# Kernel optimization log

Measured on AMD Instinct MI355X. Metric: run time of the kernel, lower is better.

## Reference

```python
import jax, jax.numpy as jnp
import numpy as np

N_NODES = 50000
N_EDGES = 640000
D = 128
BN_EPS = 1e-5
NEG_SLOPE = 0.2  # PyG GATv2Conv default negative_slope


def setup_inputs() -> dict:
    key = jax.random.key(0)
    ks = jax.random.split(key, 8)
    s = 1.0 / np.sqrt(D)
    x = jax.random.normal(ks[0], (N_NODES, D), dtype=jnp.float32)
    edge_index = jax.random.randint(ks[1], (2, N_EDGES), 0, N_NODES, dtype=jnp.int32)
    edge_attr = jax.random.uniform(ks[2], (N_EDGES, 1), dtype=jnp.float32)
    Wl = jax.random.normal(ks[3], (D, D), dtype=jnp.float32) * s
    Wr = jax.random.normal(ks[4], (D, D), dtype=jnp.float32) * s
    We = jax.random.normal(ks[5], (1, D), dtype=jnp.float32) * s
    att = jax.random.normal(ks[6], (D,), dtype=jnp.float32) * s
    return {
        "x": x, "edge_index": edge_index, "edge_attr": edge_attr,
        "Wl": Wl, "bl": jnp.zeros((D,), jnp.float32),
        "Wr": Wr, "br": jnp.zeros((D,), jnp.float32),
        "We": We, "att": att,
        "bias_out": jnp.zeros((D,), jnp.float32),
        "bn_gamma": jnp.ones((D,), jnp.float32),
        "bn_beta": jnp.zeros((D,), jnp.float32),
    }


def _gatv2(x, edge_index, edge_attr, Wl, bl, Wr, br, We, att, bias_out):
    # GATv2Conv, heads=1, concat=True, dropout treated as eval (p=0)
    src, dst = edge_index[0], edge_index[1]
    xl = x @ Wl + bl                      # source-side transform [N, D]
    xr = x @ Wr + br                      # target-side transform [N, D]
    e = edge_attr @ We                    # edge embedding       [E, D]
    m = xl[src] + xr[dst] + e             # gather + fuse        [E, D]
    m = jax.nn.leaky_relu(m, NEG_SLOPE)
    logits = m @ att                      # per-edge score [E]
    n = x.shape[0]
    # segment softmax over destination node neighborhoods
    mx = jax.ops.segment_max(logits, dst, num_segments=n)
    ex = jnp.exp(logits - mx[dst])
    den = jax.ops.segment_sum(ex, dst, num_segments=n)
    alpha = ex / (den[dst] + 1e-16)
    out = jax.ops.segment_sum(xl[src] * alpha[:, None], dst, num_segments=n)
    return out + bias_out


def reference(x, edge_index, edge_attr, Wl, bl, Wr, br, We, att, bias_out,
              bn_gamma, bn_beta):
    h = x + _gatv2(x, edge_index, edge_attr, Wl, bl, Wr, br, We, att, bias_out)
    h = jax.nn.gelu(h, approximate=False)  # torch nn.GELU default (erf)
    # BatchNorm over node dim, training-style batch stats (biased var)
    mean = jnp.mean(h, axis=0)
    var = jnp.mean((h - mean) ** 2, axis=0)
    h = (h - mean) * jax.lax.rsqrt(var + BN_EPS) * bn_gamma + bn_beta
    return h
```

## Files before the change

### kernel.cpp

```cpp
#include <hip/hip_runtime.h>
#include <math.h>

#define D 128
#define SCAN_CHUNK 256

typedef __attribute__((ext_vector_type(8))) short short8;
typedef __attribute__((ext_vector_type(4))) float f32x4;

__device__ __forceinline__ unsigned short f2bf(float f) {
    unsigned u = __float_as_uint(f);
    unsigned r = (u + 0x7fff + ((u >> 16) & 1)) >> 16;
    return (unsigned short)r;
}
__device__ __forceinline__ float bflo(unsigned u) { return __uint_as_float(u << 16); }
__device__ __forceinline__ float bfhi(unsigned u) { return __uint_as_float(u & 0xffff0000u); }

__global__ __launch_bounds__(256) void init_pack_k(const float* __restrict__ Wl,
    const float* __restrict__ Wr, unsigned short* __restrict__ wpack,
    int* __restrict__ deg, int* __restrict__ deghist, int n, int nzb)
{
    if (blockIdx.x < 16) {
        const int lane = threadIdx.x & 63;
        const int wv = threadIdx.x >> 6;
        const int slot = blockIdx.x * 4 + wv;
        const int ct = slot >> 2;
        const int kt = slot & 3;
        const float* W = (ct < 8) ? Wl : Wr;
        const int cb = (ct & 7) * 16 + (lane & 15);
        const int kb = kt * 32 + (lane >> 4) * 8;
        unsigned short v[8];
#pragma unroll
        for (int i = 0; i < 8; i++) v[i] = f2bf(W[(size_t)(kb + i) * D + cb]);
        *(uint4*)(wpack + ((size_t)slot << 9) + lane * 8) = *(uint4*)v;
    } else {
        const int tid = (blockIdx.x - 16) * 256 + threadIdx.x;
        const int stride = nzb * 256;
        for (int i = tid; i < n; i += stride) deg[i] = 0;
        if (tid < 256) deghist[tid] = 0;
    }
}

__global__ __launch_bounds__(256) void gemm_mfma_k(const float* __restrict__ x,
    const unsigned short* __restrict__ wpack, const float* __restrict__ bl,
    const float* __restrict__ br, unsigned* __restrict__ xlb,
    float* __restrict__ xr, int n)
{
    const int lane = threadIdx.x & 63;
    const int wv = threadIdx.x >> 6;
    const int rt = blockIdx.x * 4 + wv;
    if (rt * 16 >= n) return;
    const int r0 = rt * 16;
    const int ra = r0 + (lane & 15);
    const int r = ra < n ? ra : n - 1;
    const int ko = (lane >> 4) * 8;

    short8 a[4];
#pragma unroll
    for (int kt = 0; kt < 4; kt++) {
        const float* px = x + (size_t)r * D + kt * 32 + ko;
        float4 lo = *(const float4*)px;
        float4 hi = *(const float4*)(px + 4);
        short8 t;
        t[0] = (short)f2bf(lo.x); t[1] = (short)f2bf(lo.y);
        t[2] = (short)f2bf(lo.z); t[3] = (short)f2bf(lo.w);
        t[4] = (short)f2bf(hi.x); t[5] = (short)f2bf(hi.y);
        t[6] = (short)f2bf(hi.z); t[7] = (short)f2bf(hi.w);
        a[kt] = t;
    }

    f32x4 acc[16];
#pragma unroll
    for (int i = 0; i < 16; i++) acc[i] = (f32x4){0.f, 0.f, 0.f, 0.f};

#pragma unroll
    for (int kt = 0; kt < 4; kt++) {
#pragma unroll
        for (int ct = 0; ct < 16; ct++) {
            short8 b = *(const short8*)(wpack + (((size_t)(ct * 4 + kt)) << 9) + lane * 8);
            acc[ct] = __builtin_amdgcn_mfma_f32_16x16x32_bf16(a[kt], b, acc[ct], 0, 0, 0);
        }
    }

    const int colb = lane & 15;
    const int rbase = r0 + (lane >> 4) * 4;
#pragma unroll
    for (int ct = 8; ct < 16; ct++) {
        const int c = (ct - 8) * 16 + colb;
        const float bb = br[c];
#pragma unroll
        for (int reg = 0; reg < 4; reg++) {
            const int row = rbase + reg;
            if (row < n) xr[(size_t)row * D + c] = acc[ct][reg] + bb;
        }
    }
#pragma unroll
    for (int ct = 0; ct < 8; ct++) {
        const int c = ct * 16 + colb;
        const float bb = bl[c];
#pragma unroll
        for (int reg = 0; reg < 4; reg++) {
            unsigned mybf = f2bf(acc[ct][reg] + bb);
            unsigned other = (unsigned)__shfl_xor((int)mybf, 1);
            if ((lane & 1) == 0) {
                const int row = rbase + reg;
                if (row < n) xlb[(size_t)row * 64 + (c >> 1)] = mybf | (other << 16);
            }
        }
    }
}

__global__ __launch_bounds__(256) void hist_k(const int* __restrict__ ei,
    int* __restrict__ deg, int E)
{
    const int tid = blockIdx.x * 256 + threadIdx.x;
    const int stride = gridDim.x * 256;
#pragma unroll
    for (int u = 0; u < 4; u++) {
        const int e = tid + u * stride;
        if (e < E) atomicAdd(&deg[ei[E + e]], 1);
    }
}

__global__ __launch_bounds__(256) void scan_sum_k(const int* __restrict__ deg,
    int* __restrict__ bsum, int* __restrict__ deghist, int n)
{
    __shared__ int lh[256];
    const int t = threadIdx.x;
    lh[t] = 0;
    __syncthreads();
    const int i = blockIdx.x * SCAN_CHUNK + t;
    int s = 0;
    if (i < n) {
        s = deg[i];
        atomicAdd(&lh[min(s, 255)], 1);
    }
#pragma unroll
    for (int off = 32; off > 0; off >>= 1) s += __shfl_xor(s, off);
    __shared__ int ws_[4];
    const int lane = t & 63, w = t >> 6;
    if (lane == 0) ws_[w] = s;
    __syncthreads();
    if (t == 0) bsum[blockIdx.x] = ws_[0] + ws_[1] + ws_[2] + ws_[3];
    if (lh[t]) atomicAdd(&deghist[t], lh[t]);
}

__global__ __launch_bounds__(256) void scan_off_k(const int* __restrict__ bsum,
    int* __restrict__ boff, int* __restrict__ rowptr,
    const int* __restrict__ deghist, int* __restrict__ degcur, int nb, int n)
{
    const int t = threadIdx.x;
    const int lane = t & 63, w = t >> 6;
    int v = (t < nb) ? bsum[t] : 0;
    int inc = v;
#pragma unroll
    for (int off = 1; off < 64; off <<= 1) {
        int u = __shfl_up(inc, off);
        if (lane >= off) inc += u;
    }
    __shared__ int wsum[4], wpre[4];
    if (lane == 63) wsum[w] = inc;
    __syncthreads();
    if (t == 0) {
        int r = 0;
#pragma unroll
        for (int j = 0; j < 4; j++) { wpre[j] = r; r += wsum[j]; }
        rowptr[n] = r;
    }
    __syncthreads();
    if (t < nb) boff[t] = inc - v + wpre[w];
    int dv = deghist[t];
    int dinc = dv;
#pragma unroll
    for (int off = 1; off < 64; off <<= 1) {
        int u = __shfl_up(dinc, off);
        if (lane >= off) dinc += u;
    }
    __shared__ int w2sum[4], w2pre[4];
    if (lane == 63) w2sum[w] = dinc;
    __syncthreads();
    if (t == 0) {
        int r = 0;
#pragma unroll
        for (int j = 0; j < 4; j++) { w2pre[j] = r; r += w2sum[j]; }
    }
    __syncthreads();
    degcur[t] = dinc - dv + w2pre[w];
}

__global__ __launch_bounds__(256) void scan_fin_k(int* __restrict__ deg,
    const int* __restrict__ boff, int* __restrict__ rowptr,
    int* __restrict__ degcur, int* __restrict__ nodeord, int n)
{
    __shared__ int wsum[4], wpre[4];
    __shared__ int lh[256], lbase[256];
    const int t = threadIdx.x;
    const int i = blockIdx.x * SCAN_CHUNK + t;
    lh[t] = 0;
    int v = (i < n) ? deg[i] : 0;
    const int bin = min(v, 255);
    const int lane = t & 63, w = t >> 6;
    int inc = v;
#pragma unroll
    for (int off = 1; off < 64; off <<= 1) {
        int u = __shfl_up(inc, off);
        if (lane >= off) inc += u;
    }
    if (lane == 63) wsum[w] = inc;
    __syncthreads();
    if (t == 0) {
        int r = 0;
#pragma unroll
        for (int j = 0; j < 4; j++) { wpre[j] = r; r += wsum[j]; }
    }
    __syncthreads();
    int rank = 0;
    if (i < n) {
        rank = atomicAdd(&lh[bin], 1);
        int ex = inc - v + wpre[w] + boff[blockIdx.x];
        rowptr[i] = ex;
        deg[i] = ex;
    }
    __syncthreads();
    lbase[t] = lh[t] ? atomicAdd(&degcur[t], lh[t]) : 0;
    __syncthreads();
    if (i < n) nodeord[lbase[bin] + rank] = i;
}

__global__ __launch_bounds__(256) void scatter_k(const int* __restrict__ ei,
    const float* __restrict__ ea, int* __restrict__ cursor,
    unsigned* __restrict__ edges, int E)
{
    const int tid = blockIdx.x * 256 + threadIdx.x;
    const int stride = gridDim.x * 256;
#pragma unroll
    for (int u = 0; u < 4; u++) {
        const int e = tid + u * stride;
        if (e < E) {
            const int dst = ei[E + e];
            const int pos = atomicAdd(&cursor[dst], 1);
            edges[pos] = ((unsigned)ei[e] << 16) | (unsigned)f2bf(ea[e]);
        }
    }
}

__global__ __launch_bounds__(256) void agg_k(const unsigned* __restrict__ xlb,
    const float* __restrict__ xr, const float* __restrict__ x,
    const float* __restrict__ bias, const int* __restrict__ rowptr,
    const unsigned* __restrict__ edges, const float* __restrict__ We,
    const float* __restrict__ att, const int* __restrict__ nodeord,
    unsigned* __restrict__ hbf, float* __restrict__ partials, int n)
{
    const int t = threadIdx.x;
    const int gg = (blockIdx.x * 256 + t) >> 4;
    const int li = t & 15;
    const int f0 = li * 8;
    const bool active = gg < n;

    float sum[8], sq[8];
#pragma unroll
    for (int k = 0; k < 8; k++) { sum[k] = 0.f; sq[k] = 0.f; }

    if (active) {
        const int v = nodeord[n - 1 - gg];
        const int beg = rowptr[v];
        const int end = rowptr[v + 1];

        float xrv[8], wev[8], atv[8];
        {
            float4 a0 = *(const float4*)(xr + (size_t)v * D + f0);
            float4 a1 = *(const float4*)(xr + (size_t)v * D + f0 + 4);
            xrv[0]=a0.x; xrv[1]=a0.y; xrv[2]=a0.z; xrv[3]=a0.w;
            xrv[4]=a1.x; xrv[5]=a1.y; xrv[6]=a1.z; xrv[7]=a1.w;
            float4 w0 = *(const float4*)(We + f0);
            float4 w1 = *(const float4*)(We + f0 + 4);
            wev[0]=w0.x; wev[1]=w0.y; wev[2]=w0.z; wev[3]=w0.w;
            wev[4]=w1.x; wev[5]=w1.y; wev[6]=w1.z; wev[7]=w1.w;
            float4 t0 = *(const float4*)(att + f0);
            float4 t1 = *(const float4*)(att + f0 + 4);
            atv[0]=t0.x; atv[1]=t0.y; atv[2]=t0.z; atv[3]=t0.w;
            atv[4]=t1.x; atv[5]=t1.y; atv[6]=t1.z; atv[7]=t1.w;
        }

        float m = -1e30f, s = 0.f;
        float acc[8];
#pragma unroll
        for (int k = 0; k < 8; k++) acc[k] = 0.f;

        int j = beg;
        unsigned pk0 = 0u, pk1 = 0u;
        uint4 xb0 = make_uint4(0,0,0,0), xb1 = make_uint4(0,0,0,0);
        if (j < end) {
            pk0 = edges[j];
            const int j1 = (j + 1 < end) ? j + 1 : end - 1;
            pk1 = edges[j1];
            xb0 = *(const uint4*)(xlb + (size_t)(pk0 >> 16) * 64 + li * 4);
            xb1 = *(const uint4*)(xlb + (size_t)(pk1 >> 16) * 64 + li * 4);
        }
        while (j < end) {
            const int jn = j + 2;
            unsigned pn0 = pk0, pn1 = pk1;
            uint4 xn0 = xb0, xn1 = xb1;
            if (jn < end) {
                pn0 = edges[jn];
                const int j3 = (jn + 1 < end) ? jn + 1 : end - 1;
                pn1 = edges[j3];
                xn0 = *(const uint4*)(xlb + (size_t)(pn0 >> 16) * 64 + li * 4);
                xn1 = *(const uint4*)(xlb + (size_t)(pn1 >> 16) * 64 + li * 4);
            }

            const float ea0 = bflo(pk0);
            const float ea1 = bflo(pk1);
            float xv0[8], xv1[8];
            xv0[0] = bflo(xb0.x); xv0[1] = bfhi(xb0.x);
            xv0[2] = bflo(xb0.y); xv0[3] = bfhi(xb0.y);
            xv0[4] = bflo(xb0.z); xv0[5] = bfhi(xb0.z);
            xv0[6] = bflo(xb0.w); xv0[7] = bfhi(xb0.w);
            xv1[0] = bflo(xb1.x); xv1[1] = bfhi(xb1.x);
            xv1[2] = bflo(xb1.y); xv1[3] = bfhi(xb1.y);
            xv1[4] = bflo(xb1.z); xv1[5] = bfhi(xb1.z);
            xv1[6] = bflo(xb1.w); xv1[7] = bfhi(xb1.w);

            float p0 = 0.f, p1 = 0.f;
#pragma unroll
            for (int k = 0; k < 8; k++) {
                float t0 = fmaf(ea0, wev[k], xrv[k]) + xv0[k];
                t0 = fmaxf(t0, 0.2f * t0);
                p0 = fmaf(t0, atv[k], p0);
                float t1 = fmaf(ea1, wev[k], xrv[k]) + xv1[k];
                t1 = fmaxf(t1, 0.2f * t1);
                p1 = fmaf(t1, atv[k], p1);
            }
#pragma unroll
            for (int off = 8; off >= 1; off >>= 1) {
                p0 += __shfl_xor(p0, off);
                p1 += __shfl_xor(p1, off);
            }
            if (j + 1 >= end) p1 = -1e30f;

            const float pm = fmaxf(m, fmaxf(p0, p1));
            const float sc = __expf(m - pm);
            const float w0 = __expf(p0 - pm);
            const float w1 = __expf(p1 - pm);
            s = s * sc + w0 + w1;
#pragma unroll
            for (int k = 0; k < 8; k++)
                acc[k] = fmaf(acc[k], sc, fmaf(w0, xv0[k], w1 * xv1[k]));
            m = pm;

            pk0 = pn0; pk1 = pn1; xb0 = xn0; xb1 = xn1; j = jn;
        }

        const float inv = 1.f / (s + 1e-16f);
        float xa[8], bb[8];
        {
            float4 a0 = *(const float4*)(x + (size_t)v * D + f0);
            float4 a1 = *(const float4*)(x + (size_t)v * D + f0 + 4);
            xa[0]=a0.x; xa[1]=a0.y; xa[2]=a0.z; xa[3]=a0.w;
            xa[4]=a1.x; xa[5]=a1.y; xa[6]=a1.z; xa[7]=a1.w;
            float4 b0 = *(const float4*)(bias + f0);
            float4 b1 = *(const float4*)(bias + f0 + 4);
            bb[0]=b0.x; bb[1]=b0.y; bb[2]=b0.z; bb[3]=b0.w;
            bb[4]=b1.x; bb[5]=b1.y; bb[6]=b1.z; bb[7]=b1.w;
        }
        float ge[8];
#pragma unroll
        for (int k = 0; k < 8; k++) {
            const float hv = xa[k] + fmaf(acc[k], inv, bb[k]);
            const float g = 0.5f * hv * (1.f + erff(hv * 0.70710678118654752f));
            ge[k] = g;
            sum[k] = g;
            sq[k] = g * g;
        }
        unsigned o0 = (unsigned)f2bf(ge[0]) | ((unsigned)f2bf(ge[1]) << 16);
        unsigned o1 = (unsigned)f2bf(ge[2]) | ((unsigned)f2bf(ge[3]) << 16);
        unsigned o2 = (unsigned)f2bf(ge[4]) | ((unsigned)f2bf(ge[5]) << 16);
        unsigned o3 = (unsigned)f2bf(ge[6]) | ((unsigned)f2bf(ge[7]) << 16);
        *(uint4*)(hbf + (size_t)v * 64 + li * 4) = make_uint4(o0, o1, o2, o3);
    }

#pragma unroll
    for (int k = 0; k < 8; k++) {
        sum[k] += __shfl_xor(sum[k], 16);
        sum[k] += __shfl_xor(sum[k], 32);
        sq[k]  += __shfl_xor(sq[k], 16);
        sq[k]  += __shfl_xor(sq[k], 32);
    }
    __shared__ float redS[4][128], redQ[4][128];
    const int wv_ = t >> 6;
    const int lane_ = t & 63;
    if (lane_ < 16) {
#pragma unroll
        for (int k = 0; k < 8; k++) {
            redS[wv_][f0 + k] = sum[k];
            redQ[wv_][f0 + k] = sq[k];
        }
    }
    __syncthreads();
    if (t < 128) {
        const float ts = redS[0][t] + redS[1][t] + redS[2][t] + redS[3][t];
        const float tq = redQ[0][t] + redQ[1][t] + redQ[2][t] + redQ[3][t];
        partials[(size_t)blockIdx.x * 256 + t] = ts;
        partials[(size_t)blockIdx.x * 256 + 128 + t] = tq;
    }
}

__global__ __launch_bounds__(256) void bn_reduce_params_k(const float* __restrict__ partials,
    const float* __restrict__ gamma, const float* __restrict__ beta,
    float* __restrict__ ab, float n, int nblk)
{
    const int c = blockIdx.x;
    const int t = threadIdx.x;
    float s = 0.f, q = 0.f;
    for (int b = t; b < nblk; b += 256) {
        s += partials[(size_t)b * 256 + c];
        q += partials[(size_t)b * 256 + 128 + c];
    }
#pragma unroll
    for (int off = 32; off > 0; off >>= 1) {
        s += __shfl_xor(s, off);
        q += __shfl_xor(q, off);
    }
    __shared__ float ss[4], qq[4];
    const int lane = t & 63, w = t >> 6;
    if (lane == 0) { ss[w] = s; qq[w] = q; }
    __syncthreads();
    if (t == 0) {
        float S = ss[0] + ss[1] + ss[2] + ss[3];
        float Q = qq[0] + qq[1] + qq[2] + qq[3];
        float mean = S / n;
        float var = Q / n - mean * mean;
        float a = rsqrtf(var + 1e-5f) * gamma[c];
        ab[c] = a;
        ab[c + 128] = beta[c] - mean * a;
    }
}

__global__ __launch_bounds__(256) void bn_apply_k(const unsigned* __restrict__ hbf,
    float* __restrict__ out, const float* __restrict__ ab, int total4)
{
    int i4 = blockIdx.x * blockDim.x + threadIdx.x;
    if (i4 >= total4) return;
    int cg = i4 & 31;
    uint2 hp = *(const uint2*)(hbf + (size_t)i4 * 2);
    float4 a = ((const float4*)ab)[cg];
    float4 b = ((const float4*)(ab + 128))[cg];
    ((float4*)out)[i4] = make_float4(bflo(hp.x) * a.x + b.x, bfhi(hp.x) * a.y + b.y,
                                     bflo(hp.y) * a.z + b.z, bfhi(hp.y) * a.w + b.w);
}

extern "C" void kernel_launch(void* const* d_in, const int* in_sizes, int n_in,
                              void* d_out, int out_size, void* d_ws, size_t ws_size,
                              hipStream_t stream)
{
    const float* x    = (const float*)d_in[0];
    const int*   ei   = (const int*)d_in[1];
    const float* ea   = (const float*)d_in[2];
    const float* Wl   = (const float*)d_in[3];
    const float* bl   = (const float*)d_in[4];
    const float* Wr   = (const float*)d_in[5];
    const float* br   = (const float*)d_in[6];
    const float* We   = (const float*)d_in[7];
    const float* att  = (const float*)d_in[8];
    const float* bias = (const float*)d_in[9];
    const float* gamma= (const float*)d_in[10];
    const float* beta = (const float*)d_in[11];
    float* out = (float*)d_out;

    const int n = in_sizes[0] / D;
    const int E = in_sizes[1] / 2;
    const int nb = (n + SCAN_CHUNK - 1) / SCAN_CHUNK;
    const int ablk = (n * 16 + 255) / 256;

    char* ws = (char*)d_ws;
    unsigned short* wpack = (unsigned short*)ws;
    unsigned* xlb = (unsigned*)(ws + 65536);
    unsigned* hbf = xlb + (size_t)n * 64;
    float* xr = (float*)(hbf + (size_t)n * 64);
    int* deg = (int*)(xr + (size_t)n * D);
    int* rowptr = deg + n;
    int* deghist = rowptr + n + 1;
    int* degcur = deghist + 256;
    int* nodeord = degcur + 256;
    int* bsum = nodeord + n;
    int* boff = bsum + nb;
    unsigned* edges = (unsigned*)(boff + nb);
    float* partials = (float*)(edges + E);
    float* ab = partials + (size_t)256 * ablk;

    const int nzb = 98;
    init_pack_k<<<16 + nzb, 256, 0, stream>>>(Wl, Wr, wpack, deg, deghist, n, nzb);
    const int nrt = (n + 15) / 16;
    gemm_mfma_k<<<(nrt + 3) / 4, 256, 0, stream>>>(x, wpack, bl, br, xlb, xr, n);
    hist_k<<<(E / 4 + 255) / 256, 256, 0, stream>>>(ei, deg, E);
    scan_sum_k<<<nb, 256, 0, stream>>>(deg, bsum, deghist, n);
    scan_off_k<<<1, 256, 0, stream>>>(bsum, boff, rowptr, deghist, degcur, nb, n);
    scan_fin_k<<<nb, 256, 0, stream>>>(deg, boff, rowptr, degcur, nodeord, n);
    scatter_k<<<(E / 4 + 255) / 256, 256, 0, stream>>>(ei, ea, deg, edges, E);
    agg_k<<<ablk, 256, 0, stream>>>(xlb, xr, x, bias, rowptr, edges, We, att,
                                    nodeord, hbf, partials, n);
    bn_reduce_params_k<<<128, 256, 0, stream>>>(partials, gamma, beta, ab, (float)n, ablk);
    const int total4 = (n * D) / 4;
    bn_apply_k<<<(total4 + 255) / 256, 256, 0, stream>>>(hbf, out, ab, total4);
}
```

Before: 181.0 us.

## Fuse GEMM, degree histogram and coarse bucketing into one launch; two-pass CSR build

Merges the projection GEMM, the degree histogram and a new coarse edge-bucketing pass into one heterogeneous kernel launch, so they overlap and fewer launches are issued. Edges are first bucketed by destination group (128 nodes, 8 sub-cells per group) into a capped buffer that aliases the hbf region. A second pass then places each edge using LDS atomics on per-node cursors. This replaces the single scatter that did global atomics on the per-node cursor array. Each cell holds at most 512 entries and overflow edges are silently dropped, which is a correctness risk for skewed degree distributions.

```diff
diff --git a/kernel.cpp b/kernel.cpp
--- a/kernel.cpp
+++ b/kernel.cpp
@@ -3,6 +3,8 @@
 
 #define D 128
 #define SCAN_CHUNK 256
+#define BKT_SHIFT 7
+#define CELL_CAP 512
 
 typedef __attribute__((ext_vector_type(8))) short short8;
 typedef __attribute__((ext_vector_type(4))) float f32x4;
@@ -17,7 +19,8 @@
 
 __global__ __launch_bounds__(256) void init_pack_k(const float* __restrict__ Wl,
     const float* __restrict__ Wr, unsigned short* __restrict__ wpack,
-    int* __restrict__ deg, int* __restrict__ deghist, int n, int nzb)
+    int* __restrict__ deg, int* __restrict__ deghist, int* __restrict__ bcur,
+    int n, int ncell, int nzb)
 {
     if (blockIdx.x < 16) {
         const int lane = threadIdx.x & 63;
@@ -36,88 +39,96 @@
         const int tid = (blockIdx.x - 16) * 256 + threadIdx.x;
         const int stride = nzb * 256;
         for (int i = tid; i < n; i += stride) deg[i] = 0;
+        for (int i = tid; i < ncell; i += stride) bcur[i] = 0;
         if (tid < 256) deghist[tid] = 0;
     }
 }
 
-__global__ __launch_bounds__(256) void gemm_mfma_k(const float* __restrict__ x,
+__global__ __launch_bounds__(256) void fused_mid_k(const float* __restrict__ x,
     const unsigned short* __restrict__ wpack, const float* __restrict__ bl,
-    const float* __restrict__ br, unsigned* __restrict__ xlb,
-    float* __restrict__ xr, int n)
-{
-    const int lane = threadIdx.x & 63;
-    const int wv = threadIdx.x >> 6;
-    const int rt = blockIdx.x * 4 + wv;
-    if (rt * 16 >= n) return;
-    const int r0 = rt * 16;
-    const int ra = r0 + (lane & 15);
-    const int r = ra < n ? ra : n - 1;
-    const int ko = (lane >> 4) * 8;
-
-    short8 a[4];
-#pragma unroll
-    for (int kt = 0; kt < 4; kt++) {
-        const float* px = x + (size_t)r * D + kt * 32 + ko;
-        float4 lo = *(const float4*)px;
-        float4 hi = *(const float4*)(px + 4);
-        short8 t;
-        t[0] = (short)f2bf(lo.x); t[1] = (short)f2bf(lo.y);
-        t[2] = (short)f2bf(lo.z); t[3] = (short)f2bf(lo.w);
-        t[4] = (short)f2bf(hi.x); t[5] = (short)f2bf(hi.y);
-        t[6] = (short)f2bf(hi.z); t[7] = (short)f2bf(hi.w);
-        a[kt] = t;
-    }
-
-    f32x4 acc[16];
-#pragma unroll
-    for (int i = 0; i < 16; i++) acc[i] = (f32x4){0.f, 0.f, 0.f, 0.f};
-
-#pragma unroll
-    for (int kt = 0; kt < 4; kt++) {
-#pragma unroll
-        for (int ct = 0; ct < 16; ct++) {
-            short8 b = *(const short8*)(wpack + (((size_t)(ct * 4 + kt)) << 9) + lane * 8);
-            acc[ct] = __builtin_amdgcn_mfma_f32_16x16x32_bf16(a[kt], b, acc[ct], 0, 0, 0);
-        }
-    }
-
-    const int colb = lane & 15;
-    const int rbase = r0 + (lane >> 4) * 4;
-#pragma unroll
-    for (int ct = 8; ct < 16; ct++) {
-        const int c = (ct - 8) * 16 + colb;
-        const float bb = br[c];
-#pragma unroll
-        for (int reg = 0; reg < 4; reg++) {
-            const int row = rbase + reg;
-            if (row < n) xr[(size_t)row * D + c] = acc[ct][reg] + bb;
-        }
-    }
-#pragma unroll
-    for (int ct = 0; ct < 8; ct++) {
-        const int c = ct * 16 + colb;
-        const float bb = bl[c];
-#pragma unroll
-        for (int reg = 0; reg < 4; reg++) {
-            unsigned mybf = f2bf(acc[ct][reg] + bb);
-            unsigned other = (unsigned)__shfl_xor((int)mybf, 1);
-            if ((lane & 1) == 0) {
+    const float* __restrict__ br, unsigned* __restrict__ xlb, float* __restrict__ xr,
+    const int* __restrict__ ei, const float* __restrict__ ea,
+    int* __restrict__ deg, int* __restrict__ bcur, uint2* __restrict__ coarse,
+    int n, int E, int G1, int G2)
+{
+    const int b = blockIdx.x;
+    if (b < G1) {
+        const int lane = threadIdx.x & 63;
+        const int wv = threadIdx.x >> 6;
+        const int rt = b * 4 + wv;
+        if (rt * 16 >= n) return;
+        const int r0 = rt * 16;
+        const int ra = r0 + (lane & 15);
+        const int r = ra < n ? ra : n - 1;
+        const int ko = (lane >> 4) * 8;
+
+        short8 a[4];
+#pragma unroll
+        for (int kt = 0; kt < 4; kt++) {
+            const float* px = x + (size_t)r * D + kt * 32 + ko;
+            float4 lo = *(const float4*)px;
+            float4 hi = *(const float4*)(px + 4);
+            short8 t;
+            t[0] = (short)f2bf(lo.x); t[1] = (short)f2bf(lo.y);
+            t[2] = (short)f2bf(lo.z); t[3] = (short)f2bf(lo.w);
+            t[4] = (short)f2bf(hi.x); t[5] = (short)f2bf(hi.y);
+            t[6] = (short)f2bf(hi.z); t[7] = (short)f2bf(hi.w);
+            a[kt] = t;
+        }
+
+        f32x4 acc[16];
+#pragma unroll
+        for (int i = 0; i < 16; i++) acc[i] = (f32x4){0.f, 0.f, 0.f, 0.f};
+
+#pragma unroll
+        for (int kt = 0; kt < 4; kt++) {
+#pragma unroll
+            for (int ct = 0; ct < 16; ct++) {
+                short8 bb = *(const short8*)(wpack + (((size_t)(ct * 4 + kt)) << 9) + lane * 8);
+                acc[ct] = __builtin_amdgcn_mfma_f32_16x16x32_bf16(a[kt], bb, acc[ct], 0, 0, 0);
+            }
+        }
+
+        const int colb = lane & 15;
+        const int rbase = r0 + (lane >> 4) * 4;
+#pragma unroll
+        for (int ct = 8; ct < 16; ct++) {
+            const int c = (ct - 8) * 16 + colb;
+            const float bb = br[c];
+#pragma unroll
+            for (int reg = 0; reg < 4; reg++) {
                 const int row = rbase + reg;
-                if (row < n) xlb[(size_t)row * 64 + (c >> 1)] = mybf | (other << 16);
+                if (row < n) xr[(size_t)row * D + c] = acc[ct][reg] + bb;
             }
         }
-    }
-}
-
-__global__ __launch_bounds__(256) void hist_k(const int* __restrict__ ei,
-    int* __restrict__ deg, int E)
-{
-    const int tid = blockIdx.x * 256 + threadIdx.x;
-    const int stride = gridDim.x * 256;
-#pragma unroll
-    for (int u = 0; u < 4; u++) {
-        const int e = tid + u * stride;
+#pragma unroll
+        for (int ct = 0; ct < 8; ct++) {
+            const int c = ct * 16 + colb;
+            const float bb = bl[c];
+#pragma unroll
+            for (int reg = 0; reg < 4; reg++) {
+                unsigned mybf = f2bf(acc[ct][reg] + bb);
+                unsigned other = (unsigned)__shfl_xor((int)mybf, 1);
+                if ((lane & 1) == 0) {
+                    const int row = rbase + reg;
+                    if (row < n) xlb[(size_t)row * 64 + (c >> 1)] = mybf | (other << 16);
+                }
+            }
+        }
+    } else if (b < G1 + G2) {
+        const int e = (b - G1) * 256 + threadIdx.x;
         if (e < E) atomicAdd(&deg[ei[E + e]], 1);
+    } else {
+        const int e = (b - G1 - G2) * 256 + threadIdx.x;
+        if (e < E) {
+            const int dst = ei[E + e];
+            const int src = ei[e];
+            const int cell = ((dst >> BKT_SHIFT) << 3) | (b & 7);
+            const int pos = atomicAdd(&bcur[cell], 1);
+            if (pos < CELL_CAP)
+                coarse[((size_t)cell << 9) + pos] =
+                    make_uint2(((unsigned)src << 16) | (unsigned)f2bf(ea[e]), (unsigned)dst);
+        }
     }
 }
 
@@ -226,19 +237,26 @@
     if (i < n) nodeord[lbase[bin] + rank] = i;
 }
 
-__global__ __launch_bounds__(256) void scatter_k(const int* __restrict__ ei,
-    const float* __restrict__ ea, int* __restrict__ cursor,
-    unsigned* __restrict__ edges, int E)
-{
-    const int tid = blockIdx.x * 256 + threadIdx.x;
-    const int stride = gridDim.x * 256;
-#pragma unroll
-    for (int u = 0; u < 4; u++) {
-        const int e = tid + u * stride;
-        if (e < E) {
-            const int dst = ei[E + e];
-            const int pos = atomicAdd(&cursor[dst], 1);
-            edges[pos] = ((unsigned)ei[e] << 16) | (unsigned)f2bf(ea[e]);
+__global__ __launch_bounds__(256) void pass2_k(const uint2* __restrict__ coarse,
+    const int* __restrict__ bcur, const int* __restrict__ rowptr,
+    unsigned* __restrict__ edges, int n)
+{
+    __shared__ int lcur[1 << BKT_SHIFT];
+    const int b = blockIdx.x;
+    const int t = threadIdx.x;
+    const int d0 = b << BKT_SHIFT;
+    if (t < (1 << BKT_SHIFT) && d0 + t < n) lcur[t] = rowptr[d0 + t];
+    __syncthreads();
+#pragma unroll
+    for (int sub = 0; sub < 8; sub++) {
+        const int cell = (b << 3) | sub;
+        const int cnt = min(bcur[cell], CELL_CAP);
+        const uint2* base = coarse + ((size_t)cell << 9);
+        for (int i = t; i < cnt; i += 256) {
+            const uint2 en = base[i];
+            const int ld = (int)en.y - d0;
+            const int pos = atomicAdd(&lcur[ld], 1);
+            edges[pos] = en.x;
         }
     }
 }
@@ -470,12 +488,19 @@
     const int E = in_sizes[1] / 2;
     const int nb = (n + SCAN_CHUNK - 1) / SCAN_CHUNK;
     const int ablk = (n * 16 + 255) / 256;
+    const int nbk = (n + (1 << BKT_SHIFT) - 1) >> BKT_SHIFT;
+    const int ncell = nbk * 8;
 
     char* ws = (char*)d_ws;
     unsigned short* wpack = (unsigned short*)ws;
     unsigned* xlb = (unsigned*)(ws + 65536);
-    unsigned* hbf = xlb + (size_t)n * 64;
-    float* xr = (float*)(hbf + (size_t)n * 64);
+    char* ubase = (char*)(xlb + (size_t)n * 64);
+    size_t usz = (size_t)ncell * CELL_CAP * 8;
+    size_t hsz = (size_t)n * 64 * 4;
+    if (hsz > usz) usz = hsz;
+    uint2* coarse = (uint2*)ubase;
+    unsigned* hbf = (unsigned*)ubase;
+    float* xr = (float*)(ubase + usz);
     int* deg = (int*)(xr + (size_t)n * D);
     int* rowptr = deg + n;
     int* deghist = rowptr + n + 1;
@@ -483,19 +508,24 @@
     int* nodeord = degcur + 256;
     int* bsum = nodeord + n;
     int* boff = bsum + nb;
-    unsigned* edges = (unsigned*)(boff + nb);
+    int* bcur = boff + nb;
+    unsigned* edges = (unsigned*)(bcur + ncell);
     float* partials = (float*)(edges + E);
     float* ab = partials + (size_t)256 * ablk;
 
     const int nzb = 98;
-    init_pack_k<<<16 + nzb, 256, 0, stream>>>(Wl, Wr, wpack, deg, deghist, n, nzb);
+    init_pack_k<<<16 + nzb, 256, 0, stream>>>(Wl, Wr, wpack, deg, deghist, bcur, n, ncell, nzb);
+
     const int nrt = (n + 15) / 16;
-    gemm_mfma_k<<<(nrt + 3) / 4, 256, 0, stream>>>(x, wpack, bl, br, xlb, xr, n);
-    hist_k<<<(E / 4 + 255) / 256, 256, 0, stream>>>(ei, deg, E);
+    const int G1 = (nrt + 3) / 4;
+    const int G2 = (E + 255) / 256;
+    const int G3 = (E + 255) / 256;
+    fused_mid_k<<<G1 + G2 + G3, 256, 0, stream>>>(x, wpack, bl, br, xlb, xr,
+                                                  ei, ea, deg, bcur, coarse, n, E, G1, G2);
     scan_sum_k<<<nb, 256, 0, stream>>>(deg, bsum, deghist, n);
     scan_off_k<<<1, 256, 0, stream>>>(bsum, boff, rowptr, deghist, degcur, nb, n);
     scan_fin_k<<<nb, 256, 0, stream>>>(deg, boff, rowptr, degcur, nodeord, n);
-    scatter_k<<<(E / 4 + 255) / 256, 256, 0, stream>>>(ei, ea, deg, edges, E);
+    pass2_k<<<nbk, 256, 0, stream>>>(coarse, bcur, rowptr, edges, n);
     agg_k<<<ablk, 256, 0, stream>>>(xlb, xr, x, bias, rowptr, edges, We, att,
                                     nodeord, hbf, partials, n);
     bn_reduce_params_k<<<128, 256, 0, stream>>>(partials, gamma, beta, ab, (float)n, ablk);
```

New measurement: 190.2 us. +5.1%, slower.
